# Performance work log

Measured on AMD Instinct MI355X. Metric: run time of the kernel, lower is better.

The kernel has to match this reference:

```python
import jax, jax.numpy as jnp
import numpy as np

N_NODES = 50000
N_EDGES = 400000
D = 64        # hidden_features
H_NE = 16     # hidden_ne_features
L = 4         # num_layers
EPS = 1e-5


def _ln(z, g, b):
    # layer norm over feature dim
    mu = jnp.mean(z, axis=-1, keepdims=True)
    var = jnp.var(z, axis=-1, keepdims=True)
    return (z - mu) * jax.lax.rsqrt(var + EPS) * g + b


def setup_inputs() -> dict:
    key = jax.random.key(0)
    ks = iter(jax.random.split(key, 64))
    def rn(shape, s=0.05):
        return jax.random.normal(next(ks), shape, dtype=jnp.float32) * s
    inp = {
        "x": rn((N_NODES, 2), 1.0),
        "e": rn((N_EDGES, 2), 1.0),
        "src": jax.random.randint(next(ks), (N_EDGES,), 0, N_NODES, dtype=jnp.int32),
        "dst": jax.random.randint(next(ks), (N_EDGES,), 0, N_NODES, dtype=jnp.int32),
        # node / edge encoders (2-layer MLPs)
        "ne_W1": rn((2, H_NE)), "ne_b1": jnp.zeros((H_NE,), jnp.float32),
        "ne_W2": rn((H_NE, D)), "ne_b2": jnp.zeros((D,), jnp.float32),
        "ee_W1": rn((2, H_NE)), "ee_b1": jnp.zeros((H_NE,), jnp.float32),
        "ee_W2": rn((H_NE, D)), "ee_b2": jnp.zeros((D,), jnp.float32),
        # stacked per-layer GatedGCN weights
        "A1": rn((L, D, D)), "bA1": jnp.zeros((L, D), jnp.float32),
        "A2": rn((L, D, D)), "bA2": jnp.zeros((L, D), jnp.float32),
        "A3": rn((L, D, D)), "bA3": jnp.zeros((L, D), jnp.float32),
        "B1": rn((L, D, D)), "bB1": jnp.zeros((L, D), jnp.float32),
        "B2": rn((L, D, D)), "bB2": jnp.zeros((L, D), jnp.float32),
        "B3": rn((L, D, D)), "bB3": jnp.zeros((L, D), jnp.float32),
        "ge": jnp.ones((L, D), jnp.float32), "be": jnp.zeros((L, D), jnp.float32),
        "gh": jnp.ones((L, D), jnp.float32), "bh": jnp.zeros((L, D), jnp.float32),
        # score predictor
        "pW1": rn((3 * D, D)), "pb1": jnp.zeros((D,), jnp.float32),
        "pW2": rn((D, 1)), "pb2": jnp.zeros((1,), jnp.float32),
    }
    return inp


def _forward(x, e, src, dst,
             ne_W1, ne_b1, ne_W2, ne_b2,
             ee_W1, ee_b1, ee_W2, ee_b2,
             A1, bA1, A2, bA2, A3, bA3,
             B1, bB1, B2, bB2, B3, bB3,
             ge, be, gh, bh,
             pW1, pb1, pW2, pb2):
    # encoders
    x = jax.nn.relu(x @ ne_W1 + ne_b1) @ ne_W2 + ne_b2      # [N, D]
    e = jax.nn.relu(e @ ee_W1 + ee_b1) @ ee_W2 + ee_b2      # [E, D]

    params = {"A1": A1, "bA1": bA1, "A2": A2, "bA2": bA2,
              "A3": A3, "bA3": bA3, "B1": B1, "bB1": bB1,
              "B2": B2, "bB2": bB2, "B3": B3, "bB3": bB3,
              "ge": ge, "be": be, "gh": gh, "bh": bh}

    def layer(carry, p):
        x, e = carry
        # edge update: e_ij += ReLU(LN(B1 h_i + B2 h_j + B3 e_ij))
        e_hat = (x[src] @ p["B1"] + p["bB1"]
                 + x[dst] @ p["B2"] + p["bB2"]
                 + e @ p["B3"] + p["bB3"])                  # [E, D]
        e = e + jax.nn.relu(_ln(e_hat, p["ge"], p["be"]))
        sigma = jax.nn.sigmoid(e)                             # gates [E, D]
        # directed aggregation: forward (src->dst) and backward (dst->src)
        a2 = x @ p["A2"] + p["bA2"]
        a3 = x @ p["A3"] + p["bA3"]
        m_f = jax.ops.segment_sum(sigma * a2[src], dst, num_segments=N_NODES)
        d_f = jax.ops.segment_sum(sigma, dst, num_segments=N_NODES)
        m_b = jax.ops.segment_sum(sigma * a3[dst], src, num_segments=N_NODES)
        d_b = jax.ops.segment_sum(sigma, src, num_segments=N_NODES)
        h = (x @ p["A1"] + p["bA1"]
             + m_f / (d_f + EPS) + m_b / (d_b + EPS))        # [N, D]
        x = x + jax.nn.relu(_ln(h, p["gh"], p["bh"]))
        return (x, e), None

    (x, e), _ = jax.lax.scan(layer, (x, e), params)

    # score predictor: MLP over cat(x_src, x_dst, e)
    z = jnp.concatenate([x[src], x[dst], e], axis=-1)        # [E, 3D]
    return jax.nn.relu(z @ pW1 + pb1) @ pW2 + pb2            # [E, 1]


def reference(x, e, src, dst,
              ne_W1, ne_b1, ne_W2, ne_b2,
              ee_W1, ee_b1, ee_W2, ee_b2,
              A1, bA1, A2, bA2, A3, bA3,
              B1, bB1, B2, bB2, B3, bB3,
              ge, be, gh, bh,
              pW1, pb1, pW2, pb2):
    return _forward(x, e, src, dst,
                    ne_W1, ne_b1, ne_W2, ne_b2,
                    ee_W1, ee_b1, ee_W2, ee_b2,
                    A1, bA1, A2, bA2, A3, bA3,
                    B1, bB1, B2, bB2, B3, bB3,
                    ge, be, gh, bh,
                    pW1, pb1, pW2, pb2)
```

## Files before the change

kernel.cpp:

```cpp
#include <hip/hip_runtime.h>

#define N_NODES 50000
#define N_EDGES 400000
#define EPSV 1e-5f
#define SCAN_BLK 49
#define SCAN_PAD (49 * 1024)

__global__ __launch_bounds__(256) void encode_kernel(
    const float* __restrict__ in2, const float* __restrict__ W1,
    const float* __restrict__ b1, const float* __restrict__ W2,
    const float* __restrict__ b2, float* __restrict__ out, int nrows)
{
  int t = blockIdx.x * 256 + threadIdx.x;
  int row = t >> 4;
  int d0 = t & 15;
  if (row >= nrows) return;
  float x0 = in2[row * 2 + 0], x1 = in2[row * 2 + 1];
  float h[16];
#pragma unroll
  for (int j = 0; j < 16; ++j)
    h[j] = fmaxf(fmaf(x0, W1[j], fmaf(x1, W1[16 + j], b1[j])), 0.f);
#pragma unroll
  for (int q = 0; q < 4; ++q) {
    int d = d0 + q * 16;
    float a = b2[d];
#pragma unroll
    for (int j = 0; j < 16; ++j) a = fmaf(h[j], W2[j * 64 + d], a);
    out[(size_t)row * 64 + d] = a;
  }
}

__global__ __launch_bounds__(256) void hist_kernel(
    const int* __restrict__ src, const int* __restrict__ dst,
    int* __restrict__ cnt_f, int* __restrict__ cnt_b)
{
  int t = blockIdx.x * 256 + threadIdx.x;
  if (t >= N_EDGES) return;
  atomicAdd(&cnt_f[dst[t]], 1);
  atomicAdd(&cnt_b[src[t]], 1);
}

__global__ __launch_bounds__(1024) void scanA_kernel(
    const int* __restrict__ cnt_f, const int* __restrict__ cnt_b,
    int* __restrict__ part, int* __restrict__ bsum)
{
  int dir = blockIdx.x / SCAN_BLK;
  int blk = blockIdx.x % SCAN_BLK;
  const int* cnt = dir ? cnt_b : cnt_f;
  int t = threadIdx.x;
  int idx = blk * 1024 + t;
  int v = (idx < N_NODES) ? cnt[idx] : 0;
  __shared__ int sh[1024];
  sh[t] = v;
  __syncthreads();
  for (int o = 1; o < 1024; o <<= 1) {
    int u = (t >= o) ? sh[t - o] : 0;
    __syncthreads();
    sh[t] += u;
    __syncthreads();
  }
  part[dir * SCAN_PAD + idx] = sh[t] - v;
  if (t == 1023) bsum[dir * SCAN_BLK + blk] = sh[1023];
}

__global__ __launch_bounds__(64) void scanB_kernel(
    int* __restrict__ bsum, int* __restrict__ off_f, int* __restrict__ off_b)
{
  int t = threadIdx.x;
  if (t < 2) {
    int* b = bsum + t * SCAN_BLK;
    int run = 0;
    for (int i = 0; i < SCAN_BLK; ++i) {
      int v = b[i];
      b[i] = run;
      run += v;
    }
    if (t == 0) off_f[N_NODES] = run;
    else off_b[N_NODES] = run;
  }
}

__global__ __launch_bounds__(1024) void scanC_kernel(
    const int* __restrict__ part, const int* __restrict__ bsum,
    int* __restrict__ off_f, int* __restrict__ off_b,
    int* __restrict__ cur_f, int* __restrict__ cur_b)
{
  int dir = blockIdx.x / SCAN_BLK;
  int blk = blockIdx.x % SCAN_BLK;
  int t = threadIdx.x;
  int idx = blk * 1024 + t;
  if (idx >= N_NODES) return;
  int v = part[dir * SCAN_PAD + idx] + bsum[dir * SCAN_BLK + blk];
  if (dir == 0) { off_f[idx] = v; cur_f[idx] = v; }
  else { off_b[idx] = v; cur_b[idx] = v; }
}

__global__ __launch_bounds__(256) void fill_kernel(
    const int* __restrict__ src, const int* __restrict__ dst,
    int* __restrict__ cur_f, int* __restrict__ cur_b,
    int2* __restrict__ csr_f, int2* __restrict__ csr_b)
{
  int t = blockIdx.x * 256 + threadIdx.x;
  if (t >= N_EDGES) return;
  int dv = dst[t], sv = src[t];
  int p = atomicAdd(&cur_f[dv], 1);
  csr_f[p] = make_int2(t, sv);
  int q = atomicAdd(&cur_b[sv], 1);
  csr_b[q] = make_int2(t, dv);
}

__global__ __launch_bounds__(256) void sort_kernel(
    const int* __restrict__ off_f, const int* __restrict__ off_b,
    int2* __restrict__ csr_f, int2* __restrict__ csr_b)
{
  int t = blockIdx.x * 256 + threadIdx.x;
  int n;
  int2* csr;
  const int* off;
  if (t < N_NODES) { n = t; csr = csr_f; off = off_f; }
  else if (t < 2 * N_NODES) { n = t - N_NODES; csr = csr_b; off = off_b; }
  else return;
  int b = off[n], e = off[n + 1];
  for (int i = b + 1; i < e; ++i) {
    int2 key = csr[i];
    int j = i - 1;
    while (j >= b && csr[j].x > key.x) { csr[j + 1] = csr[j]; --j; }
    csr[j + 1] = key;
  }
}


__global__ __launch_bounds__(256, 3) void node_gemm_kernel(
    const float* __restrict__ X,
    const float* __restrict__ A1, const float* __restrict__ A2,
    const float* __restrict__ A3, const float* __restrict__ B1,
    const float* __restrict__ B2,
    const float* __restrict__ bA1, const float* __restrict__ bA2,
    const float* __restrict__ bA3, const float* __restrict__ bB1,
    const float* __restrict__ bB2,
    float* __restrict__ NA, int l)
{
  __shared__ float ett[4][64 * 36];
  const int NT = 1563;
  int wid = threadIdx.x >> 6;
  int lane = threadIdx.x & 63;
  int wf = blockIdx.x * 4 + wid;
  if (wf >= 5 * NT) return;
  int m = wf / NT;
  int t = wf - m * NT;
  int row0 = t * 32;
  int r8 = lane & 7, c8 = lane >> 3;
  int col = 8 * c8;
  float* tl = ett[wid];
#pragma unroll
  for (int rb = 0; rb < 8; ++rb) {
    int r = row0 + 4 * rb;
    float v0 = (r + 0 < N_NODES) ? X[(size_t)(r + 0) * 64 + lane] : 0.f;
    float v1 = (r + 1 < N_NODES) ? X[(size_t)(r + 1) * 64 + lane] : 0.f;
    float v2 = (r + 2 < N_NODES) ? X[(size_t)(r + 2) * 64 + lane] : 0.f;
    float v3 = (r + 3 < N_NODES) ? X[(size_t)(r + 3) * 64 + lane] : 0.f;
    *reinterpret_cast<float4*>(&tl[lane * 36 + 4 * rb]) =
        make_float4(v0, v1, v2, v3);
  }
  const float* W;
  const float* bb;
  if (m == 0) { W = A1; bb = bA1; }
  else if (m == 1) { W = A2; bb = bA2; }
  else if (m == 2) { W = A3; bb = bA3; }
  else if (m == 3) { W = B1; bb = bB1; }
  else { W = B2; bb = bB2; }
  W += l * 64 * 64;
  float acc[4][8];
#pragma unroll
  for (int i = 0; i < 4; ++i)
#pragma unroll
    for (int j = 0; j < 8; ++j) acc[i][j] = 0.f;
#pragma unroll 8
  for (int k = 0; k < 64; ++k) {
    float4 er = *reinterpret_cast<const float4*>(&tl[k * 36 + 4 * r8]);
    float4 w0 = *reinterpret_cast<const float4*>(&W[k * 64 + col]);
    float4 w1 = *reinterpret_cast<const float4*>(&W[k * 64 + col + 4]);
    float ev[4] = {er.x, er.y, er.z, er.w};
    float wv[8] = {w0.x, w0.y, w0.z, w0.w, w1.x, w1.y, w1.z, w1.w};
#pragma unroll
    for (int i = 0; i < 4; ++i)
#pragma unroll
      for (int j = 0; j < 8; ++j) acc[i][j] = fmaf(ev[i], wv[j], acc[i][j]);
  }
  float4 b0 = *reinterpret_cast<const float4*>(&bb[l * 64 + col]);
  float4 b1 = *reinterpret_cast<const float4*>(&bb[l * 64 + col + 4]);
  float* out = NA + (size_t)m * N_NODES * 64;
#pragma unroll
  for (int i = 0; i < 4; ++i) {
    int row = row0 + 4 * r8 + i;
    if (row < N_NODES) {
      *reinterpret_cast<float4*>(&out[(size_t)row * 64 + col]) =
          make_float4(acc[i][0] + b0.x, acc[i][1] + b0.y, acc[i][2] + b0.z,
                      acc[i][3] + b0.w);
      *reinterpret_cast<float4*>(&out[(size_t)row * 64 + col + 4]) =
          make_float4(acc[i][4] + b1.x, acc[i][5] + b1.y, acc[i][6] + b1.z,
                      acc[i][7] + b1.w);
    }
  }
}

__global__ __launch_bounds__(256, 3) void edge_update_kernel(
    const float* __restrict__ NA,
    const float* __restrict__ B3, const float* __restrict__ bB3,
    const float* __restrict__ ge, const float* __restrict__ be,
    const int* __restrict__ src, const int* __restrict__ dst,
    float* __restrict__ E64, int l)
{
  __shared__ float ett[4][64 * 36];
  int wid = threadIdx.x >> 6;
  int lane = threadIdx.x & 63;
  int tile = blockIdx.x * 4 + wid;
  int e0 = tile * 32;
  int r8 = lane & 7, c8 = lane >> 3;
  int col = 8 * c8;
  float* tl = ett[wid];
#pragma unroll
  for (int rb = 0; rb < 8; ++rb) {
    int r = e0 + 4 * rb;
    float v0 = E64[(size_t)(r + 0) * 64 + lane];
    float v1 = E64[(size_t)(r + 1) * 64 + lane];
    float v2 = E64[(size_t)(r + 2) * 64 + lane];
    float v3 = E64[(size_t)(r + 3) * 64 + lane];
    *reinterpret_cast<float4*>(&tl[lane * 36 + 4 * rb]) =
        make_float4(v0, v1, v2, v3);
  }
  const float* W = B3 + l * 64 * 64;
  float acc[4][8];
#pragma unroll
  for (int i = 0; i < 4; ++i)
#pragma unroll
    for (int j = 0; j < 8; ++j) acc[i][j] = 0.f;
#pragma unroll 8
  for (int k = 0; k < 64; ++k) {
    float4 er = *reinterpret_cast<const float4*>(&tl[k * 36 + 4 * r8]);
    float4 w0 = *reinterpret_cast<const float4*>(&W[k * 64 + col]);
    float4 w1 = *reinterpret_cast<const float4*>(&W[k * 64 + col + 4]);
    float ev[4] = {er.x, er.y, er.z, er.w};
    float wv[8] = {w0.x, w0.y, w0.z, w0.w, w1.x, w1.y, w1.z, w1.w};
#pragma unroll
    for (int i = 0; i < 4; ++i)
#pragma unroll
      for (int j = 0; j < 8; ++j) acc[i][j] = fmaf(ev[i], wv[j], acc[i][j]);
  }
  const float* b1x = NA + (size_t)3 * N_NODES * 64;
  const float* b2x = NA + (size_t)4 * N_NODES * 64;
  float4 t0, t1;
  t0 = *reinterpret_cast<const float4*>(&bB3[l * 64 + col]);
  t1 = *reinterpret_cast<const float4*>(&bB3[l * 64 + col + 4]);
  float bbv[8] = {t0.x, t0.y, t0.z, t0.w, t1.x, t1.y, t1.z, t1.w};
  t0 = *reinterpret_cast<const float4*>(&ge[l * 64 + col]);
  t1 = *reinterpret_cast<const float4*>(&ge[l * 64 + col + 4]);
  float gev[8] = {t0.x, t0.y, t0.z, t0.w, t1.x, t1.y, t1.z, t1.w};
  t0 = *reinterpret_cast<const float4*>(&be[l * 64 + col]);
  t1 = *reinterpret_cast<const float4*>(&be[l * 64 + col + 4]);
  float bev[8] = {t0.x, t0.y, t0.z, t0.w, t1.x, t1.y, t1.z, t1.w};
#pragma unroll
  for (int i = 0; i < 4; ++i) {
    int row = e0 + 4 * r8 + i;
    int sv = src[row], dv = dst[row];
    float4 g0 = *reinterpret_cast<const float4*>(&b1x[(size_t)sv * 64 + col]);
    float4 g1 = *reinterpret_cast<const float4*>(&b1x[(size_t)sv * 64 + col + 4]);
    float4 h0 = *reinterpret_cast<const float4*>(&b2x[(size_t)dv * 64 + col]);
    float4 h1 = *reinterpret_cast<const float4*>(&b2x[(size_t)dv * 64 + col + 4]);
    float4 o0 = *reinterpret_cast<const float4*>(&E64[(size_t)row * 64 + col]);
    float4 o1 = *reinterpret_cast<const float4*>(&E64[(size_t)row * 64 + col + 4]);
    float g1v[8] = {g0.x, g0.y, g0.z, g0.w, g1.x, g1.y, g1.z, g1.w};
    float g2v[8] = {h0.x, h0.y, h0.z, h0.w, h1.x, h1.y, h1.z, h1.w};
    float eov[8] = {o0.x, o0.y, o0.z, o0.w, o1.x, o1.y, o1.z, o1.w};
    float z[8];
    float s1 = 0.f, s2 = 0.f;
#pragma unroll
    for (int j = 0; j < 8; ++j) {
      z[j] = acc[i][j] + bbv[j] + g1v[j] + g2v[j];
      s1 += z[j];
      s2 = fmaf(z[j], z[j], s2);
    }
    s1 += __shfl_xor(s1, 8, 64);  s2 += __shfl_xor(s2, 8, 64);
    s1 += __shfl_xor(s1, 16, 64); s2 += __shfl_xor(s2, 16, 64);
    s1 += __shfl_xor(s1, 32, 64); s2 += __shfl_xor(s2, 32, 64);
    float mean = s1 * (1.f / 64.f);
    float var = fmaxf(s2 * (1.f / 64.f) - mean * mean, 0.f);
    float rstd = rsqrtf(var + EPSV);
    float o[8];
#pragma unroll
    for (int j = 0; j < 8; ++j)
      o[j] = eov[j] + fmaxf(fmaf((z[j] - mean) * rstd, gev[j], bev[j]), 0.f);
    *reinterpret_cast<float4*>(&E64[(size_t)row * 64 + col]) =
        make_float4(o[0], o[1], o[2], o[3]);
    *reinterpret_cast<float4*>(&E64[(size_t)row * 64 + col + 4]) =
        make_float4(o[4], o[5], o[6], o[7]);
  }
}

__global__ __launch_bounds__(256) void aggregate_kernel(
    const float* __restrict__ NA, const float* __restrict__ E64,
    const int* __restrict__ off_f, const int* __restrict__ off_b,
    const int2* __restrict__ csr_f, const int2* __restrict__ csr_b,
    const float* __restrict__ gh, const float* __restrict__ bh,
    float* __restrict__ X, int l)
{
  int wave = threadIdx.x >> 6;
  int lane = threadIdx.x & 63;
  int n = blockIdx.x * 4 + wave;
  if (n >= N_NODES) return;
  const float* A1x = NA;
  const float* A2x = NA + (size_t)N_NODES * 64;
  const float* A3x = NA + (size_t)2 * N_NODES * 64;
  float xo = X[(size_t)n * 64 + lane];
  float a1v = A1x[(size_t)n * 64 + lane];
  float ghv = gh[l * 64 + lane];
  float bhv = bh[l * 64 + lane];
  int pf = off_f[n], pfe = off_f[n + 1];
  int pb = off_b[n], pbe = off_b[n + 1];
  float mf = 0.f, df = 0.f, mb = 0.f, db = 0.f;
  bool hf = pf < pfe, hb = pb < pbe;
  float evf = 0.f, avf = 0.f, evb = 0.f, avb = 0.f;
  if (hf) {
    int2 c = csr_f[pf];
    evf = E64[(size_t)c.x * 64 + lane];
    avf = A2x[(size_t)c.y * 64 + lane];
  }
  if (hb) {
    int2 c = csr_b[pb];
    evb = E64[(size_t)c.x * 64 + lane];
    avb = A3x[(size_t)c.y * 64 + lane];
  }
  while (hf || hb) {
    bool nf = (pf + 1) < pfe;
    bool nb = (pb + 1) < pbe;
    float evf2 = 0.f, avf2 = 0.f, evb2 = 0.f, avb2 = 0.f;
    if (nf) {
      int2 c = csr_f[pf + 1];
      evf2 = E64[(size_t)c.x * 64 + lane];
      avf2 = A2x[(size_t)c.y * 64 + lane];
    }
    if (nb) {
      int2 c = csr_b[pb + 1];
      evb2 = E64[(size_t)c.x * 64 + lane];
      avb2 = A3x[(size_t)c.y * 64 + lane];
    }
    if (hf) {
      float sg = __builtin_amdgcn_rcpf(1.f + __expf(-evf));
      mf = fmaf(sg, avf, mf);
      df += sg;
      ++pf;
      evf = evf2;
      avf = avf2;
      hf = nf;
    }
    if (hb) {
      float sg = __builtin_amdgcn_rcpf(1.f + __expf(-evb));
      mb = fmaf(sg, avb, mb);
      db += sg;
      ++pb;
      evb = evb2;
      avb = avb2;
      hb = nb;
    }
  }
  float h = a1v + mf * __builtin_amdgcn_rcpf(df + EPSV) +
            mb * __builtin_amdgcn_rcpf(db + EPSV);
  float s1 = h, s2 = h * h;
#pragma unroll
  for (int m = 1; m < 64; m <<= 1) {
    s1 += __shfl_xor(s1, m, 64);
    s2 += __shfl_xor(s2, m, 64);
  }
  float mean = s1 * (1.f / 64.f);
  float var = fmaxf(s2 * (1.f / 64.f) - mean * mean, 0.f);
  float rstd = rsqrtf(var + EPSV);
  X[(size_t)n * 64 + lane] =
      xo + fmaxf(fmaf((h - mean) * rstd, ghv, bhv), 0.f);
}

__global__ __launch_bounds__(256, 3) void pred_node_kernel(
    const float* __restrict__ X, const float* __restrict__ pW1,
    float* __restrict__ U, float* __restrict__ V)
{
  __shared__ float ett[4][64 * 36];
  const int NT = 1563;
  int wid = threadIdx.x >> 6;
  int lane = threadIdx.x & 63;
  int wf = blockIdx.x * 4 + wid;
  if (wf >= 2 * NT) return;
  int m = wf / NT;
  int t = wf - m * NT;
  int row0 = t * 32;
  int r8 = lane & 7, c8 = lane >> 3;
  int col = 8 * c8;
  float* tl = ett[wid];
#pragma unroll
  for (int rb = 0; rb < 8; ++rb) {
    int r = row0 + 4 * rb;
    float v0 = (r + 0 < N_NODES) ? X[(size_t)(r + 0) * 64 + lane] : 0.f;
    float v1 = (r + 1 < N_NODES) ? X[(size_t)(r + 1) * 64 + lane] : 0.f;
    float v2 = (r + 2 < N_NODES) ? X[(size_t)(r + 2) * 64 + lane] : 0.f;
    float v3 = (r + 3 < N_NODES) ? X[(size_t)(r + 3) * 64 + lane] : 0.f;
    *reinterpret_cast<float4*>(&tl[lane * 36 + 4 * rb]) =
        make_float4(v0, v1, v2, v3);
  }
  const float* W = pW1 + (size_t)m * 64 * 64;
  float acc[4][8];
#pragma unroll
  for (int i = 0; i < 4; ++i)
#pragma unroll
    for (int j = 0; j < 8; ++j) acc[i][j] = 0.f;
#pragma unroll 8
  for (int k = 0; k < 64; ++k) {
    float4 er = *reinterpret_cast<const float4*>(&tl[k * 36 + 4 * r8]);
    float4 w0 = *reinterpret_cast<const float4*>(&W[k * 64 + col]);
    float4 w1 = *reinterpret_cast<const float4*>(&W[k * 64 + col + 4]);
    float ev[4] = {er.x, er.y, er.z, er.w};
    float wv[8] = {w0.x, w0.y, w0.z, w0.w, w1.x, w1.y, w1.z, w1.w};
#pragma unroll
    for (int i = 0; i < 4; ++i)
#pragma unroll
      for (int j = 0; j < 8; ++j) acc[i][j] = fmaf(ev[i], wv[j], acc[i][j]);
  }
  float* out = m ? V : U;
#pragma unroll
  for (int i = 0; i < 4; ++i) {
    int row = row0 + 4 * r8 + i;
    if (row < N_NODES) {
      *reinterpret_cast<float4*>(&out[(size_t)row * 64 + col]) =
          make_float4(acc[i][0], acc[i][1], acc[i][2], acc[i][3]);
      *reinterpret_cast<float4*>(&out[(size_t)row * 64 + col + 4]) =
          make_float4(acc[i][4], acc[i][5], acc[i][6], acc[i][7]);
    }
  }
}

__global__ __launch_bounds__(256, 3) void pred_edge_kernel(
    const float* __restrict__ U, const float* __restrict__ V,
    const float* __restrict__ E64,
    const int* __restrict__ src, const int* __restrict__ dst,
    const float* __restrict__ pW1, const float* __restrict__ pb1,
    const float* __restrict__ pW2, const float* __restrict__ pb2,
    float* __restrict__ out)
{
  __shared__ float ett[4][64 * 36];
  int wid = threadIdx.x >> 6;
  int lane = threadIdx.x & 63;
  int tile = blockIdx.x * 4 + wid;
  int e0 = tile * 32;
  int r8 = lane & 7, c8 = lane >> 3;
  int col = 8 * c8;
  float* tl = ett[wid];
#pragma unroll
  for (int rb = 0; rb < 8; ++rb) {
    int r = e0 + 4 * rb;
    float v0 = E64[(size_t)(r + 0) * 64 + lane];
    float v1 = E64[(size_t)(r + 1) * 64 + lane];
    float v2 = E64[(size_t)(r + 2) * 64 + lane];
    float v3 = E64[(size_t)(r + 3) * 64 + lane];
    *reinterpret_cast<float4*>(&tl[lane * 36 + 4 * rb]) =
        make_float4(v0, v1, v2, v3);
  }
  const float* W = pW1 + (size_t)128 * 64;
  float acc[4][8];
#pragma unroll
  for (int i = 0; i < 4; ++i)
#pragma unroll
    for (int j = 0; j < 8; ++j) acc[i][j] = 0.f;
#pragma unroll 8
  for (int k = 0; k < 64; ++k) {
    float4 er = *reinterpret_cast<const float4*>(&tl[k * 36 + 4 * r8]);
    float4 w0 = *reinterpret_cast<const float4*>(&W[k * 64 + col]);
    float4 w1 = *reinterpret_cast<const float4*>(&W[k * 64 + col + 4]);
    float ev[4] = {er.x, er.y, er.z, er.w};
    float wv[8] = {w0.x, w0.y, w0.z, w0.w, w1.x, w1.y, w1.z, w1.w};
#pragma unroll
    for (int i = 0; i < 4; ++i)
#pragma unroll
      for (int j = 0; j < 8; ++j) acc[i][j] = fmaf(ev[i], wv[j], acc[i][j]);
  }
  float4 t0, t1;
  t0 = *reinterpret_cast<const float4*>(&pb1[col]);
  t1 = *reinterpret_cast<const float4*>(&pb1[col + 4]);
  float pb1v[8] = {t0.x, t0.y, t0.z, t0.w, t1.x, t1.y, t1.z, t1.w};
  t0 = *reinterpret_cast<const float4*>(&pW2[col]);
  t1 = *reinterpret_cast<const float4*>(&pW2[col + 4]);
  float pw2v[8] = {t0.x, t0.y, t0.z, t0.w, t1.x, t1.y, t1.z, t1.w};
  float pb2v = pb2[0];
#pragma unroll
  for (int i = 0; i < 4; ++i) {
    int row = e0 + 4 * r8 + i;
    int sv = src[row], dv = dst[row];
    float4 g0 = *reinterpret_cast<const float4*>(&U[(size_t)sv * 64 + col]);
    float4 g1 = *reinterpret_cast<const float4*>(&U[(size_t)sv * 64 + col + 4]);
    float4 h0 = *reinterpret_cast<const float4*>(&V[(size_t)dv * 64 + col]);
    float4 h1 = *reinterpret_cast<const float4*>(&V[(size_t)dv * 64 + col + 4]);
    float g1v[8] = {g0.x, g0.y, g0.z, g0.w, g1.x, g1.y, g1.z, g1.w};
    float g2v[8] = {h0.x, h0.y, h0.z, h0.w, h1.x, h1.y, h1.z, h1.w};
    float hsum = 0.f;
#pragma unroll
    for (int j = 0; j < 8; ++j) {
      float z = acc[i][j] + pb1v[j] + g1v[j] + g2v[j];
      hsum = fmaf(fmaxf(z, 0.f), pw2v[j], hsum);
    }
    hsum += __shfl_xor(hsum, 8, 64);
    hsum += __shfl_xor(hsum, 16, 64);
    hsum += __shfl_xor(hsum, 32, 64);
    if (c8 == 0) out[row] = hsum + pb2v;
  }
}

extern "C" void kernel_launch(void* const* d_in, const int* in_sizes, int n_in,
                              void* d_out, int out_size, void* d_ws, size_t ws_size,
                              hipStream_t stream)
{
  const float* x = (const float*)d_in[0];
  const float* e = (const float*)d_in[1];
  const int* src = (const int*)d_in[2];
  const int* dst = (const int*)d_in[3];
  const float* neW1 = (const float*)d_in[4];
  const float* neb1 = (const float*)d_in[5];
  const float* neW2 = (const float*)d_in[6];
  const float* neb2 = (const float*)d_in[7];
  const float* eeW1 = (const float*)d_in[8];
  const float* eeb1 = (const float*)d_in[9];
  const float* eeW2 = (const float*)d_in[10];
  const float* eeb2 = (const float*)d_in[11];
  const float* A1 = (const float*)d_in[12];
  const float* bA1 = (const float*)d_in[13];
  const float* A2 = (const float*)d_in[14];
  const float* bA2 = (const float*)d_in[15];
  const float* A3 = (const float*)d_in[16];
  const float* bA3 = (const float*)d_in[17];
  const float* B1 = (const float*)d_in[18];
  const float* bB1 = (const float*)d_in[19];
  const float* B2 = (const float*)d_in[20];
  const float* bB2 = (const float*)d_in[21];
  const float* B3 = (const float*)d_in[22];
  const float* bB3 = (const float*)d_in[23];
  const float* ge = (const float*)d_in[24];
  const float* be = (const float*)d_in[25];
  const float* gh = (const float*)d_in[26];
  const float* bh = (const float*)d_in[27];
  const float* pW1 = (const float*)d_in[28];
  const float* pb1 = (const float*)d_in[29];
  const float* pW2 = (const float*)d_in[30];
  const float* pb2 = (const float*)d_in[31];

  char* ws = (char*)d_ws;
  float* X = (float*)ws;      ws += (size_t)N_NODES * 64 * 4;
  float* NA = (float*)ws;     ws += (size_t)5 * N_NODES * 64 * 4;
  float* E64 = (float*)ws;    ws += (size_t)N_EDGES * 64 * 4;
  int* cnt_f = (int*)ws;      ws += (size_t)N_NODES * 4;
  int* cnt_b = (int*)ws;      ws += (size_t)N_NODES * 4;
  int* off_f = (int*)ws;      ws += (size_t)(N_NODES + 1) * 4;
  int* off_b = (int*)ws;      ws += (size_t)(N_NODES + 1) * 4;
  int* cur_f = (int*)ws;      ws += (size_t)N_NODES * 4;
  int* cur_b = (int*)ws;      ws += (size_t)N_NODES * 4;
  int2* csr_f = (int2*)ws;    ws += (size_t)N_EDGES * 8;
  int2* csr_b = (int2*)ws;    ws += (size_t)N_EDGES * 8;
  int* part = (int*)ws;       ws += (size_t)2 * SCAN_PAD * 4;
  int* bsum = (int*)ws;       ws += (size_t)2 * SCAN_BLK * 4;
  float* U = NA + (size_t)3 * N_NODES * 64;
  float* V = NA + (size_t)4 * N_NODES * 64;

  encode_kernel<<<(N_NODES * 16 + 255) / 256, 256, 0, stream>>>(
      x, neW1, neb1, neW2, neb2, X, N_NODES);
  encode_kernel<<<(N_EDGES * 16 + 255) / 256, 256, 0, stream>>>(
      e, eeW1, eeb1, eeW2, eeb2, E64, N_EDGES);

  hipMemsetAsync(cnt_f, 0, (size_t)2 * N_NODES * 4, stream);
  hist_kernel<<<(N_EDGES + 255) / 256, 256, 0, stream>>>(src, dst, cnt_f, cnt_b);
  scanA_kernel<<<2 * SCAN_BLK, 1024, 0, stream>>>(cnt_f, cnt_b, part, bsum);
  scanB_kernel<<<1, 64, 0, stream>>>(bsum, off_f, off_b);
  scanC_kernel<<<2 * SCAN_BLK, 1024, 0, stream>>>(part, bsum, off_f, off_b,
                                                  cur_f, cur_b);
  fill_kernel<<<(N_EDGES + 255) / 256, 256, 0, stream>>>(src, dst, cur_f, cur_b,
                                                         csr_f, csr_b);
  sort_kernel<<<(2 * N_NODES + 255) / 256, 256, 0, stream>>>(off_f, off_b, csr_f,
                                                             csr_b);

  const int NGB = (5 * 1563 + 3) / 4;
  const int PNB = (2 * 1563 + 3) / 4;
  for (int l = 0; l < 4; ++l) {
    node_gemm_kernel<<<NGB, 256, 0, stream>>>(
        X, A1, A2, A3, B1, B2, bA1, bA2, bA3, bB1, bB2, NA, l);
    edge_update_kernel<<<N_EDGES / 128, 256, 0, stream>>>(NA, B3, bB3, ge, be,
                                                          src, dst, E64, l);
    aggregate_kernel<<<(N_NODES + 3) / 4, 256, 0, stream>>>(
        NA, E64, off_f, off_b, csr_f, csr_b, gh, bh, X, l);
  }

  pred_node_kernel<<<PNB, 256, 0, stream>>>(X, pW1, U, V);
  pred_edge_kernel<<<N_EDGES / 128, 256, 0, stream>>>(U, V, E64, src, dst, pW1,
                                                      pb1, pW2, pb2,
                                                      (float*)d_out);
}
```

Measured before the change: 1.293 ms.

## Store edge features in destination-sorted CSR order to make forward aggregation contiguous

Edge features are now encoded and stored in the order of the forward CSR, which groups edges by destination node. Forward aggregation then reads them contiguously instead of gathering them, and the destination-side lookup in the edge update becomes near-sequential. To support this, new setup kernels build an inverse permutation, a per-position destination array, and remap the backward CSR edge ids. The predictor scatters its outputs back to the original edge positions. Occupancy hints on several kernels are also raised from 3 to 4 waves, which may add register pressure.

```diff
diff --git a/kernel.cpp b/kernel.cpp
--- a/kernel.cpp
+++ b/kernel.cpp
@@ -16,6 +16,32 @@
   int d0 = t & 15;
   if (row >= nrows) return;
   float x0 = in2[row * 2 + 0], x1 = in2[row * 2 + 1];
+  float h[16];
+#pragma unroll
+  for (int j = 0; j < 16; ++j)
+    h[j] = fmaxf(fmaf(x0, W1[j], fmaf(x1, W1[16 + j], b1[j])), 0.f);
+#pragma unroll
+  for (int q = 0; q < 4; ++q) {
+    int d = d0 + q * 16;
+    float a = b2[d];
+#pragma unroll
+    for (int j = 0; j < 16; ++j) a = fmaf(h[j], W2[j * 64 + d], a);
+    out[(size_t)row * 64 + d] = a;
+  }
+}
+
+__global__ __launch_bounds__(256) void encode_perm_kernel(
+    const float* __restrict__ in2, const float* __restrict__ W1,
+    const float* __restrict__ b1, const float* __restrict__ W2,
+    const float* __restrict__ b2, const int2* __restrict__ csr_f,
+    float* __restrict__ out)
+{
+  int t = blockIdx.x * 256 + threadIdx.x;
+  int row = t >> 4;
+  int d0 = t & 15;
+  if (row >= N_EDGES) return;
+  int orig = csr_f[row].x;
+  float x0 = in2[orig * 2 + 0], x1 = in2[orig * 2 + 1];
   float h[16];
 #pragma unroll
   for (int j = 0; j < 16; ++j)
@@ -129,8 +155,34 @@
   }
 }
 
-
-__global__ __launch_bounds__(256, 3) void node_gemm_kernel(
+__global__ __launch_bounds__(256) void aux_inv_kernel(
+    const int2* __restrict__ csr_f, int* __restrict__ inv_f)
+{
+  int p = blockIdx.x * 256 + threadIdx.x;
+  if (p >= N_EDGES) return;
+  inv_f[csr_f[p].x] = p;
+}
+
+__global__ __launch_bounds__(256) void aux_dst_kernel(
+    const int* __restrict__ off_f, int* __restrict__ dst_f)
+{
+  int n = blockIdx.x * 256 + threadIdx.x;
+  if (n >= N_NODES) return;
+  int b = off_f[n], e = off_f[n + 1];
+  for (int p = b; p < e; ++p) dst_f[p] = n;
+}
+
+__global__ __launch_bounds__(256) void aux_remap_kernel(
+    const int* __restrict__ inv_f, int2* __restrict__ csr_b)
+{
+  int q = blockIdx.x * 256 + threadIdx.x;
+  if (q >= N_EDGES) return;
+  int2 c = csr_b[q];
+  csr_b[q] = make_int2(inv_f[c.x], c.y);
+}
+
+
+__global__ __launch_bounds__(256, 4) void node_gemm_kernel(
     const float* __restrict__ X,
     const float* __restrict__ A1, const float* __restrict__ A2,
     const float* __restrict__ A3, const float* __restrict__ B1,
@@ -204,11 +256,11 @@
   }
 }
 
-__global__ __launch_bounds__(256, 3) void edge_update_kernel(
+__global__ __launch_bounds__(256, 4) void edge_update_kernel(
     const float* __restrict__ NA,
     const float* __restrict__ B3, const float* __restrict__ bB3,
     const float* __restrict__ ge, const float* __restrict__ be,
-    const int* __restrict__ src, const int* __restrict__ dst,
+    const int2* __restrict__ csr_f, const int* __restrict__ dst_f,
     float* __restrict__ E64, int l)
 {
   __shared__ float ett[4][64 * 36];
@@ -262,7 +314,8 @@
 #pragma unroll
   for (int i = 0; i < 4; ++i) {
     int row = e0 + 4 * r8 + i;
-    int sv = src[row], dv = dst[row];
+    int sv = csr_f[row].y;
+    int dv = dst_f[row];
     float4 g0 = *reinterpret_cast<const float4*>(&b1x[(size_t)sv * 64 + col]);
     float4 g1 = *reinterpret_cast<const float4*>(&b1x[(size_t)sv * 64 + col + 4]);
     float4 h0 = *reinterpret_cast<const float4*>(&b2x[(size_t)dv * 64 + col]);
@@ -321,9 +374,8 @@
   bool hf = pf < pfe, hb = pb < pbe;
   float evf = 0.f, avf = 0.f, evb = 0.f, avb = 0.f;
   if (hf) {
-    int2 c = csr_f[pf];
-    evf = E64[(size_t)c.x * 64 + lane];
-    avf = A2x[(size_t)c.y * 64 + lane];
+    evf = E64[(size_t)pf * 64 + lane];
+    avf = A2x[(size_t)csr_f[pf].y * 64 + lane];
   }
   if (hb) {
     int2 c = csr_b[pb];
@@ -335,9 +387,8 @@
     bool nb = (pb + 1) < pbe;
     float evf2 = 0.f, avf2 = 0.f, evb2 = 0.f, avb2 = 0.f;
     if (nf) {
-      int2 c = csr_f[pf + 1];
-      evf2 = E64[(size_t)c.x * 64 + lane];
-      avf2 = A2x[(size_t)c.y * 64 + lane];
+      evf2 = E64[(size_t)(pf + 1) * 64 + lane];
+      avf2 = A2x[(size_t)csr_f[pf + 1].y * 64 + lane];
     }
     if (nb) {
       int2 c = csr_b[pb + 1];
@@ -378,7 +429,7 @@
       xo + fmaxf(fmaf((h - mean) * rstd, ghv, bhv), 0.f);
 }
 
-__global__ __launch_bounds__(256, 3) void pred_node_kernel(
+__global__ __launch_bounds__(256, 4) void pred_node_kernel(
     const float* __restrict__ X, const float* __restrict__ pW1,
     float* __restrict__ U, float* __restrict__ V)
 {
@@ -435,10 +486,10 @@
   }
 }
 
-__global__ __launch_bounds__(256, 3) void pred_edge_kernel(
+__global__ __launch_bounds__(256, 4) void pred_edge_kernel(
     const float* __restrict__ U, const float* __restrict__ V,
     const float* __restrict__ E64,
-    const int* __restrict__ src, const int* __restrict__ dst,
+    const int2* __restrict__ csr_f, const int* __restrict__ dst_f,
     const float* __restrict__ pW1, const float* __restrict__ pb1,
     const float* __restrict__ pW2, const float* __restrict__ pb2,
     float* __restrict__ out)
@@ -490,7 +541,9 @@
 #pragma unroll
   for (int i = 0; i < 4; ++i) {
     int row = e0 + 4 * r8 + i;
-    int sv = src[row], dv = dst[row];
+    int2 cf = csr_f[row];
+    int sv = cf.y;
+    int dv = dst_f[row];
     float4 g0 = *reinterpret_cast<const float4*>(&U[(size_t)sv * 64 + col]);
     float4 g1 = *reinterpret_cast<const float4*>(&U[(size_t)sv * 64 + col + 4]);
     float4 h0 = *reinterpret_cast<const float4*>(&V[(size_t)dv * 64 + col]);
@@ -506,7 +559,7 @@
     hsum += __shfl_xor(hsum, 8, 64);
     hsum += __shfl_xor(hsum, 16, 64);
     hsum += __shfl_xor(hsum, 32, 64);
-    if (c8 == 0) out[row] = hsum + pb2v;
+    if (c8 == 0) out[cf.x] = hsum + pb2v;
   }
 }
 
@@ -561,13 +614,10 @@
   int2* csr_b = (int2*)ws;    ws += (size_t)N_EDGES * 8;
   int* part = (int*)ws;       ws += (size_t)2 * SCAN_PAD * 4;
   int* bsum = (int*)ws;       ws += (size_t)2 * SCAN_BLK * 4;
+  int* inv_f = (int*)ws;      ws += (size_t)N_EDGES * 4;
+  int* dst_f = (int*)ws;      ws += (size_t)N_EDGES * 4;
   float* U = NA + (size_t)3 * N_NODES * 64;
   float* V = NA + (size_t)4 * N_NODES * 64;
-
-  encode_kernel<<<(N_NODES * 16 + 255) / 256, 256, 0, stream>>>(
-      x, neW1, neb1, neW2, neb2, X, N_NODES);
-  encode_kernel<<<(N_EDGES * 16 + 255) / 256, 256, 0, stream>>>(
-      e, eeW1, eeb1, eeW2, eeb2, E64, N_EDGES);
 
   hipMemsetAsync(cnt_f, 0, (size_t)2 * N_NODES * 4, stream);
   hist_kernel<<<(N_EDGES + 255) / 256, 256, 0, stream>>>(src, dst, cnt_f, cnt_b);
@@ -579,6 +629,14 @@
                                                          csr_f, csr_b);
   sort_kernel<<<(2 * N_NODES + 255) / 256, 256, 0, stream>>>(off_f, off_b, csr_f,
                                                              csr_b);
+  aux_inv_kernel<<<(N_EDGES + 255) / 256, 256, 0, stream>>>(csr_f, inv_f);
+  aux_dst_kernel<<<(N_NODES + 255) / 256, 256, 0, stream>>>(off_f, dst_f);
+  aux_remap_kernel<<<(N_EDGES + 255) / 256, 256, 0, stream>>>(inv_f, csr_b);
+
+  encode_kernel<<<(N_NODES * 16 + 255) / 256, 256, 0, stream>>>(
+      x, neW1, neb1, neW2, neb2, X, N_NODES);
+  encode_perm_kernel<<<(N_EDGES * 16 + 255) / 256, 256, 0, stream>>>(
+      e, eeW1, eeb1, eeW2, eeb2, csr_f, E64);
 
   const int NGB = (5 * 1563 + 3) / 4;
   const int PNB = (2 * 1563 + 3) / 4;
@@ -586,13 +644,13 @@
     node_gemm_kernel<<<NGB, 256, 0, stream>>>(
         X, A1, A2, A3, B1, B2, bA1, bA2, bA3, bB1, bB2, NA, l);
     edge_update_kernel<<<N_EDGES / 128, 256, 0, stream>>>(NA, B3, bB3, ge, be,
-                                                          src, dst, E64, l);
+                                                          csr_f, dst_f, E64, l);
     aggregate_kernel<<<(N_NODES + 3) / 4, 256, 0, stream>>>(
         NA, E64, off_f, off_b, csr_f, csr_b, gh, bh, X, l);
   }
 
   pred_node_kernel<<<PNB, 256, 0, stream>>>(X, pW1, U, V);
-  pred_edge_kernel<<<N_EDGES / 128, 256, 0, stream>>>(U, V, E64, src, dst, pW1,
-                                                      pb1, pW2, pb2,
+  pred_edge_kernel<<<N_EDGES / 128, 256, 0, stream>>>(U, V, E64, csr_f, dst_f,
+                                                      pW1, pb1, pW2, pb2,
                                                       (float*)d_out);
 }
```

New measurement: 1.277 ms. About the same (-1.2%).
